# Performance work log

Measured on AMD Instinct MI355X. Metric: run time of the kernel, lower is better.

## Reference

```python
import jax, jax.numpy as jnp
import numpy as np

N_TOKENS = 1024
HIDDEN = 2048
N_EXPERTS = 16
MOE_INTER = 1024
TOP_K = 6
N_GROUP = 4
TOPK_GROUP = 2
N_SHARED = 2
ROUTED_SCALING = 2.5
RENORM = True
CAPACITY = 1024  # >> N_TOKENS*TOP_K/N_EXPERTS = 384; overflow probability negligible


def setup_inputs() -> dict:
    key = jax.random.key(0)
    ks = jax.random.split(key, 7)
    s = 0.02
    return {
        'hidden_states': jax.random.normal(ks[0], (N_TOKENS, HIDDEN), jnp.float32),
        'gate_w': jax.random.normal(ks[1], (N_EXPERTS, HIDDEN), jnp.float32) * s,
        'gate_bias': jax.random.normal(ks[2], (N_EXPERTS,), jnp.float32) * s,
        'w_gate_up': jax.random.normal(ks[3], (N_EXPERTS, HIDDEN, 2 * MOE_INTER), jnp.float32) * s,
        'w_down': jax.random.normal(ks[4], (N_EXPERTS, MOE_INTER, HIDDEN), jnp.float32) * s,
        'shared_w_gate_up': jax.random.normal(ks[5], (HIDDEN, 2 * N_SHARED * MOE_INTER), jnp.float32) * s,
        'shared_w_down': jax.random.normal(ks[6], (N_SHARED * MOE_INTER, HIDDEN), jnp.float32) * s,
    }


def _swiglu(gu):
    # npu_swiglu with activate_left=True: silu(first half) * second half
    g, u = jnp.split(gu, 2, axis=-1)
    return jax.nn.silu(g) * u


def reference(hidden_states, gate_w, gate_bias, w_gate_up, w_down, shared_w_gate_up, shared_w_down):
    x = hidden_states
    N, H = x.shape
    E, K, C = N_EXPERTS, TOP_K, CAPACITY
    P = N * K  # number of (token, slot) pairs

    # ---- MoEGate: router logits + noaux_tc grouped top-k ----
    logits = x @ gate_w.T                              # [N, E]
    scores = jax.nn.sigmoid(logits)                    # sigmoid scoring (noaux_tc)
    s_corr = scores + gate_bias[None, :]
    sg = s_corr.reshape(N, N_GROUP, E // N_GROUP)
    group_scores = jax.lax.top_k(sg, 2)[0].sum(-1)     # top-2 sum per group [N, G]
    _, gidx = jax.lax.top_k(group_scores, TOPK_GROUP)
    gmask = jnp.sum(jax.nn.one_hot(gidx, N_GROUP, dtype=jnp.float32), axis=1) > 0
    masked = jnp.where(gmask[:, :, None], sg, -jnp.inf).reshape(N, E)
    _, topk_ids = jax.lax.top_k(masked, K)             # [N, K]
    w = jnp.take_along_axis(scores, topk_ids, axis=-1)  # weights from original scores
    if RENORM:
        w = w / jnp.sum(w, axis=-1, keepdims=True)
    w = w * ROUTED_SCALING

    # ---- dispatch: fixed-capacity buffers per expert ----
    flat_e = topk_ids.reshape(P)
    onehot = jax.nn.one_hot(flat_e, E, dtype=jnp.int32)
    pos = jnp.cumsum(onehot, axis=0)[jnp.arange(P), flat_e] - 1  # slot within expert
    valid = pos < C
    buf = jnp.full((E, C), P, jnp.int32).at[flat_e, jnp.clip(pos, 0, C - 1)].set(
        jnp.where(valid, jnp.arange(P, dtype=jnp.int32), P))
    tok = jnp.where(buf < P, buf // K, N)              # token index per slot, N = pad
    x_pad = jnp.concatenate([x, jnp.zeros((1, H), x.dtype)], axis=0)
    xe = x_pad[tok]                                    # [E, C, H]

    # ---- grouped expert GEMMs (SwiGLU MLP per expert) ----
    h = jnp.einsum('ech,ehi->eci', xe, w_gate_up)      # [E, C, 2I]
    y = jnp.einsum('eci,eih->ech', _swiglu(h), w_down)  # [E, C, H]

    # ---- combine: weighted scatter-add back to tokens ----
    w_pad = jnp.concatenate([w.reshape(P), jnp.zeros((1,), w.dtype)])
    pw = w_pad[jnp.where(buf < P, buf, P)]             # [E, C]
    routed = jnp.zeros((N + 1, H), x.dtype).at[tok].add(y * pw[:, :, None])[:N]

    # ---- shared experts (reduce_results=False, fused add) ----
    shared = _swiglu(x @ shared_w_gate_up) @ shared_w_down
    return routed + shared
```

## Files before the change

### kernel.cpp

```cpp
#include <hip/hip_runtime.h>
#include <hip/hip_bf16.h>
#include <math.h>

typedef __attribute__((ext_vector_type(8))) short bf16x8;
typedef __attribute__((ext_vector_type(4))) float f32x4;

#define N_TOK 1024
#define HID   2048
#define NEXP  16
#define NE2   18
#define INTER 1024
#define TOPK  6
#define CAP   1024

__device__ __forceinline__ unsigned short f2bf(float f) {
  unsigned u = __builtin_bit_cast(unsigned, f);
  u += 0x7fffu + ((u >> 16) & 1u);
  return (unsigned short)(u >> 16);
}
__device__ __forceinline__ float b2f(short s) {
  unsigned u = ((unsigned)(unsigned short)s) << 16;
  return __builtin_bit_cast(float, u);
}
__device__ __forceinline__ void gll16(const void* g, void* l) {
  __builtin_amdgcn_global_load_lds(
      (const __attribute__((address_space(1))) unsigned int*)g,
      (__attribute__((address_space(3))) unsigned int*)l, 16, 0, 0);
}
__device__ __forceinline__ void xcd_remap(int& bx, int& by, int& bz) {
  int gx = gridDim.x, gy = gridDim.y;
  int nwg = gx * gy * (int)gridDim.z;
  int lid = bx + gx * (by + gy * bz);
  int q = nwg >> 3, r = nwg & 7;
  int xcd = lid & 7, i = lid >> 3;
  int swz = (xcd < r ? xcd * (q + 1) : r * (q + 1) + (xcd - r) * q) + i;
  bx = swz % gx; int t2 = swz / gx; by = t2 % gy; bz = t2 / gy;
}

__global__ __launch_bounds__(256) void router_k(
    const float* __restrict__ x, const float* __restrict__ gw,
    const float* __restrict__ gb, int* __restrict__ counts,
    int* __restrict__ tok_list, int* __restrict__ meta,
    float* __restrict__ pwt, unsigned short* __restrict__ x_bf)
{
  const int t   = blockIdx.x;
  const int tid = threadIdx.x;
  __shared__ float xrow[HID];
  __shared__ float logits[NEXP];

  for (int i = tid; i < HID; i += 256) {
    float v = x[(size_t)t * HID + i];
    xrow[i] = v;
    x_bf[(size_t)t * HID + i] = f2bf(v);
  }
  __syncthreads();

  const int w = tid >> 6, lane = tid & 63;
  for (int s = 0; s < 4; ++s) {
    int e = w * 4 + s;
    const float* g = gw + (size_t)e * HID;
    float p = 0.f;
    for (int i = lane; i < HID; i += 64) p += xrow[i] * g[i];
    for (int off = 32; off; off >>= 1) p += __shfl_down(p, off);
    if (lane == 0) logits[e] = p;
  }
  __syncthreads();

  if (tid == 0) {
    float sc[NEXP], scorr[NEXP];
    for (int e = 0; e < NEXP; ++e) {
      float s1 = 1.f / (1.f + expf(-logits[e]));
      sc[e] = s1; scorr[e] = s1 + gb[e];
    }
    float gs[4];
    for (int g = 0; g < 4; ++g) {
      float m1 = -1e30f, m2 = -1e30f;
      for (int j = 0; j < 4; ++j) {
        float v = scorr[g * 4 + j];
        if (v > m1) { m2 = m1; m1 = v; } else if (v > m2) m2 = v;
      }
      gs[g] = m1 + m2;
    }
    int g1 = 0;
    for (int g = 1; g < 4; ++g) if (gs[g] > gs[g1]) g1 = g;
    int g2 = -1;
    for (int g = 0; g < 4; ++g) { if (g == g1) continue; if (g2 < 0 || gs[g] > gs[g2]) g2 = g; }

    bool taken[NEXP];
    for (int e = 0; e < NEXP; ++e) taken[e] = false;
    int ids[TOPK]; float wv[TOPK]; float wsum = 0.f;
    for (int k = 0; k < TOPK; ++k) {
      int best = -1; float bv = -1e30f;
      for (int e = 0; e < NEXP; ++e) {
        int grp = e >> 2;
        if (grp != g1 && grp != g2) continue;
        if (taken[e]) continue;
        if (scorr[e] > bv) { bv = scorr[e]; best = e; }
      }
      taken[best] = true; ids[k] = best; wv[k] = sc[best]; wsum += sc[best];
    }
    float inv = 2.5f / wsum;
    for (int k = 0; k < TOPK; ++k) {
      int e = ids[k];
      int slot = atomicAdd(&counts[e], 1);
      tok_list[e * CAP + slot] = t;
      meta[t * TOPK + k] = (e << 16) | slot;
      pwt[t * TOPK + k] = wv[k] * inv;
    }
  }
}

template<int MODE>
__global__ __launch_bounds__(256, 2) void gemm_fw_k(
    const unsigned short* __restrict__ A, int lda, size_t a_estride,
    const float* __restrict__ Wr, const float* __restrict__ Ws, int K,
    const int* __restrict__ counts, const int* __restrict__ tok_list,
    unsigned short* __restrict__ outb, int out_ld, size_t out_estride)
{
  int bx = blockIdx.x, by = blockIdx.y, bz = blockIdx.z;
  xcd_remap(bx, by, bz);
  const int e  = bz;
  const int m0 = by * 128;
  const int M  = (e < 16) ? counts[e] : N_TOK;
  if (m0 >= M) return;
  const int n0 = bx * (MODE == 0 ? 64 : 128);

  __shared__ __align__(16) unsigned short Al[2][128 * 64];
  __shared__ __align__(16) unsigned short Bl[2][128 * 64];

  const int tid = threadIdx.x, lane = tid & 63, wid = tid >> 6;
  const int wm = wid >> 1, wn = wid & 1, l15 = lane & 15, hi = lane >> 4;

  const unsigned short* Ap = A + (size_t)e * a_estride;

  const unsigned short* asrc[4]; int aoff[4];
  #pragma unroll
  for (int i = 0; i < 4; ++i) {
    int c = tid + 256 * i;
    int r = c >> 3, s = c & 7, sl = s ^ (r & 7);
    int slot = m0 + r;
    int row;
    if (MODE == 0) row = (e < 16) ? ((slot < M) ? tok_list[e * CAP + slot] : 0) : slot;
    else           row = slot;
    asrc[i] = Ap + (size_t)row * lda + sl * 8;
    aoff[i] = c * 16;
  }

  const int nq = tid & 31, kb8 = tid >> 5;
  const float* bp; int ldw;
  {
    int n_ = nq * 4;
    if (MODE == 0) {
      if (e < 16) {
        size_t col = (n_ < 64) ? (size_t)(n0 + n_) : (size_t)(1024 + n0 + n_ - 64);
        bp = Wr + (size_t)e * HID * (2 * INTER) + col; ldw = 2 * INTER;
      } else {
        int j = e - 16;
        size_t col = (n_ < 64) ? (size_t)(j * 1024 + n0 + n_)
                               : (size_t)(2048 + j * 1024 + n0 + n_ - 64);
        bp = Ws + col; ldw = 4096;
      }
    } else {
      bp = ((e < 16) ? Wr + (size_t)e * INTER * HID
                     : Ws + (size_t)(e - 16) * INTER * HID) + (n0 + n_);
      ldw = HID;
    }
    bp += (size_t)(kb8 * 8) * ldw;
  }
  int bwoff[4];
  #pragma unroll
  for (int j = 0; j < 4; ++j)
    bwoff[j] = (nq * 4 + j) * 128 + ((kb8 ^ (nq & 7) ^ (j << 1)) << 4);

  int bn[4];
  if (MODE == 0) { bn[0] = wn*32; bn[1] = wn*32+16; bn[2] = 64+wn*32; bn[3] = 80+wn*32; }
  else           { bn[0] = wn*64; bn[1] = wn*64+16; bn[2] = wn*64+32; bn[3] = wn*64+48; }

  f32x4 acc[4][4];
  #pragma unroll
  for (int a0 = 0; a0 < 4; ++a0)
    #pragma unroll
    for (int b0 = 0; b0 < 4; ++b0) acc[a0][b0] = (f32x4){0.f, 0.f, 0.f, 0.f};

  float4 bf4[8];
  #define LOADB(kt)                                                         \
    _Pragma("unroll")                                                       \
    for (int i = 0; i < 8; ++i)                                             \
      bf4[i] = *(const float4*)(bp + (size_t)((kt) + i) * ldw);
  #define WRITEB(Bb)                                                        \
    _Pragma("unroll")                                                       \
    for (int j = 0; j < 4; ++j) {                                           \
      unsigned w4[4];                                                       \
      _Pragma("unroll")                                                     \
      for (int q2 = 0; q2 < 4; ++q2) {                                      \
        float lo  = ((const float*)(bf4 + 2 * q2))[j];                      \
        float hi2 = ((const float*)(bf4 + 2 * q2 + 1))[j];                  \
        unsigned rr;                                                        \
        asm("v_cvt_pk_bf16_f32 %0, %1, %2" : "=v"(rr) : "v"(lo), "v"(hi2)); \
        w4[q2] = rr;                                                        \
      }                                                                     \
      *(uint4*)((char*)(Bb) + bwoff[j]) = *(uint4*)w4;                      \
    }

  LOADB(0)
  #pragma unroll
  for (int i = 0; i < 4; ++i) gll16(asrc[i], (char*)Al[0] + aoff[i]);
  asm volatile("s_waitcnt vmcnt(0)" ::: "memory");
  WRITEB(Bl[0])
  __syncthreads();

  const int nt = K >> 6;
  int p = 0;
  for (int t = 0; t < nt; ++t) {
    const bool pf = (t + 1 < nt);
    if (pf) {
      const int kt1 = (t + 1) << 6;
      #pragma unroll
      for (int i = 0; i < 4; ++i)
        gll16(asrc[i] + kt1, (char*)Al[p ^ 1] + aoff[i]);
      LOADB(kt1)
    }

    const char* Ab = (const char*)Al[p];
    const char* Bb = (const char*)Bl[p];
    #pragma unroll
    for (int kk = 0; kk < 64; kk += 32) {
      bf16x8 af[4], bv[4];
      #pragma unroll
      for (int mi = 0; mi < 4; ++mi) {
        int r = wm * 64 + mi * 16 + l15;
        int off = (r * 128 + (kk + hi * 8) * 2) ^ ((r & 7) << 4);
        af[mi] = *(const bf16x8*)(Ab + off);
      }
      #pragma unroll
      for (int ni = 0; ni < 4; ++ni) {
        int r = bn[ni] + l15;
        int slot = (kk >> 3) + hi;
        int off = r * 128 + ((slot ^ ((r >> 2) & 7) ^ ((r & 3) << 1)) << 4);
        bv[ni] = *(const bf16x8*)(Bb + off);
      }
      #pragma unroll
      for (int mi = 0; mi < 4; ++mi)
        #pragma unroll
        for (int ni = 0; ni < 4; ++ni)
          acc[mi][ni] = __builtin_amdgcn_mfma_f32_16x16x32_bf16(af[mi], bv[ni], acc[mi][ni], 0, 0, 0);
    }

    if (pf) {
      asm volatile("s_waitcnt vmcnt(0)" ::: "memory");
      WRITEB(Bl[p ^ 1])
    }
    __syncthreads();
    p ^= 1;
  }
  #undef LOADB
  #undef WRITEB

  const int rbase = hi * 4;
  if (MODE == 0) {
    #pragma unroll
    for (int mi = 0; mi < 4; ++mi)
      #pragma unroll
      for (int rr = 0; rr < 4; ++rr) {
        int slot = m0 + wm * 64 + mi * 16 + rbase + rr;
        if (slot >= M) continue;
        #pragma unroll
        for (int j = 0; j < 2; ++j) {
          float g = acc[mi][j][rr], u = acc[mi][j + 2][rr];
          float sv = g / (1.f + expf(-g)) * u;
          int col = n0 + wn * 32 + j * 16 + l15;
          outb[(size_t)e * out_estride + (size_t)slot * out_ld + col] = f2bf(sv);
        }
      }
  } else {
    #pragma unroll
    for (int mi = 0; mi < 4; ++mi)
      #pragma unroll
      for (int rr = 0; rr < 4; ++rr) {
        int slot = m0 + wm * 64 + mi * 16 + rbase + rr;
        if (slot >= M) continue;
        unsigned short* row = outb + (size_t)e * out_estride + (size_t)slot * out_ld;
        #pragma unroll
        for (int ni = 0; ni < 4; ++ni)
          row[n0 + bn[ni] + l15] = f2bf(acc[mi][ni][rr]);
      }
  }
}

__global__ __launch_bounds__(256) void combine_k(
    const unsigned short* __restrict__ ybuf, const int* __restrict__ meta,
    const float* __restrict__ pwt, float* __restrict__ out)
{
  const int t = blockIdx.x;
  const int c0 = threadIdx.x * 8;
  float acc[8];
  {
    bf16x8 v0 = *(const bf16x8*)(ybuf + ((size_t)16 * CAP + t) * HID + c0);
    bf16x8 v1 = *(const bf16x8*)(ybuf + ((size_t)17 * CAP + t) * HID + c0);
    #pragma unroll
    for (int j = 0; j < 8; ++j) acc[j] = b2f(v0[j]) + b2f(v1[j]);
  }
  #pragma unroll
  for (int k = 0; k < TOPK; ++k) {
    int m = meta[t * TOPK + k];
    float w = pwt[t * TOPK + k];
    int e = m >> 16, s = m & 0xffff;
    bf16x8 v = *(const bf16x8*)(ybuf + ((size_t)e * CAP + s) * HID + c0);
    #pragma unroll
    for (int j = 0; j < 8; ++j) acc[j] += w * b2f(v[j]);
  }
  float4* o = (float4*)(out + (size_t)t * HID + c0);
  o[0] = make_float4(acc[0], acc[1], acc[2], acc[3]);
  o[1] = make_float4(acc[4], acc[5], acc[6], acc[7]);
}

extern "C" void kernel_launch(void* const* d_in, const int* in_sizes, int n_in,
                              void* d_out, int out_size, void* d_ws, size_t ws_size,
                              hipStream_t stream) {
  const float* x   = (const float*)d_in[0];
  const float* gw  = (const float*)d_in[1];
  const float* gb  = (const float*)d_in[2];
  const float* wgu = (const float*)d_in[3];
  const float* wd  = (const float*)d_in[4];
  const float* sgu = (const float*)d_in[5];
  const float* sd  = (const float*)d_in[6];
  float* out = (float*)d_out;

  char* ws = (char*)d_ws;
  int*   counts   = (int*)ws;
  int*   tok_list = (int*)(ws + 256);
  int*   meta     = (int*)(ws + 256 + 65536);
  float* pwt      = (float*)(ws + 256 + 65536 + 24576);
  unsigned short* x_bf = (unsigned short*)(ws + 128 * 1024);
  unsigned short* act  = x_bf + (size_t)N_TOK * HID;
  unsigned short* ybuf = act + (size_t)NE2 * CAP * INTER;
  const size_t need = (size_t)((char*)(ybuf + (size_t)NE2 * CAP * HID) - ws);
  if (ws_size < need) return;

  hipMemsetAsync(counts, 0, 256, stream);
  router_k<<<N_TOK, 256, 0, stream>>>(x, gw, gb, counts, tok_list, meta, pwt, x_bf);

  gemm_fw_k<0><<<dim3(INTER / 64, CAP / 128, NE2), 256, 0, stream>>>(
      x_bf, HID, 0, wgu, sgu, HID, counts, tok_list,
      act, INTER, (size_t)CAP * INTER);
  gemm_fw_k<1><<<dim3(HID / 128, CAP / 128, NE2), 256, 0, stream>>>(
      act, INTER, (size_t)CAP * INTER, wd, sd, INTER, counts, nullptr,
      ybuf, HID, (size_t)CAP * HID);

  combine_k<<<N_TOK, 256, 0, stream>>>(ybuf, meta, pwt, out);
}
```

Before: 479.0 us.

## Deepen B-operand prefetch to two register stages with partial vmcnt waits

Restructures the GEMM main loop to keep two register buffers of fp32 B tiles in flight, loading tile t+2 while tile t+1 is converted and written to LDS. Each wait drops from vmcnt(0) to vmcnt(8), so global loads overlap the MFMA compute instead of stalling on it. The loop is unrolled by two, and sched_barriers pin the instruction order. It costs more VGPRs, which may lower occupancy, and relies on nt being even and on redundant clamped loads past the end.

```diff
diff --git a/kernel.cpp b/kernel.cpp
--- a/kernel.cpp
+++ b/kernel.cpp
@@ -182,79 +182,99 @@
     #pragma unroll
     for (int b0 = 0; b0 < 4; ++b0) acc[a0][b0] = (f32x4){0.f, 0.f, 0.f, 0.f};
 
-  float4 bf4[8];
-  #define LOADB(kt)                                                         \
+  float4 rb0[8], rb1[8];
+
+  #define LOADB(rb, kt)                                                     \
     _Pragma("unroll")                                                       \
     for (int i = 0; i < 8; ++i)                                             \
-      bf4[i] = *(const float4*)(bp + (size_t)((kt) + i) * ldw);
-  #define WRITEB(Bb)                                                        \
+      rb[i] = *(const float4*)(bp + (size_t)((kt) + i) * ldw);
+  #define WRITEB(rb, Bb)                                                    \
     _Pragma("unroll")                                                       \
     for (int j = 0; j < 4; ++j) {                                           \
       unsigned w4[4];                                                       \
       _Pragma("unroll")                                                     \
       for (int q2 = 0; q2 < 4; ++q2) {                                      \
-        float lo  = ((const float*)(bf4 + 2 * q2))[j];                      \
-        float hi2 = ((const float*)(bf4 + 2 * q2 + 1))[j];                  \
+        float lo  = ((const float*)(rb + 2 * q2))[j];                       \
+        float hi2 = ((const float*)(rb + 2 * q2 + 1))[j];                   \
         unsigned rr;                                                        \
         asm("v_cvt_pk_bf16_f32 %0, %1, %2" : "=v"(rr) : "v"(lo), "v"(hi2)); \
         w4[q2] = rr;                                                        \
       }                                                                     \
       *(uint4*)((char*)(Bb) + bwoff[j]) = *(uint4*)w4;                      \
     }
-
-  LOADB(0)
+  #define COMPUTE(Ab, Bb)                                                   \
+    _Pragma("unroll")                                                       \
+    for (int kk = 0; kk < 64; kk += 32) {                                   \
+      bf16x8 af[4], bv[4];                                                  \
+      _Pragma("unroll")                                                     \
+      for (int mi = 0; mi < 4; ++mi) {                                      \
+        int r = wm * 64 + mi * 16 + l15;                                    \
+        int off = (r * 128 + (kk + hi * 8) * 2) ^ ((r & 7) << 4);           \
+        af[mi] = *(const bf16x8*)((const char*)(Ab) + off);                 \
+      }                                                                     \
+      _Pragma("unroll")                                                     \
+      for (int ni = 0; ni < 4; ++ni) {                                      \
+        int r = bn[ni] + l15;                                               \
+        int slot = (kk >> 3) + hi;                                          \
+        int off = r * 128 + ((slot ^ ((r >> 2) & 7) ^ ((r & 3) << 1)) << 4);\
+        bv[ni] = *(const bf16x8*)((const char*)(Bb) + off);                 \
+      }                                                                     \
+      _Pragma("unroll")                                                     \
+      for (int mi = 0; mi < 4; ++mi)                                        \
+        _Pragma("unroll")                                                   \
+        for (int ni = 0; ni < 4; ++ni)                                      \
+          acc[mi][ni] = __builtin_amdgcn_mfma_f32_16x16x32_bf16(            \
+              af[mi], bv[ni], acc[mi][ni], 0, 0, 0);                        \
+    }
+
+  const int nt = K >> 6;
+  const int LT = (nt - 1) << 6;
+
+  LOADB(rb0, 0)
   #pragma unroll
   for (int i = 0; i < 4; ++i) gll16(asrc[i], (char*)Al[0] + aoff[i]);
-  asm volatile("s_waitcnt vmcnt(0)" ::: "memory");
-  WRITEB(Bl[0])
-  __syncthreads();
-
-  const int nt = K >> 6;
-  int p = 0;
-  for (int t = 0; t < nt; ++t) {
-    const bool pf = (t + 1 < nt);
-    if (pf) {
-      const int kt1 = (t + 1) << 6;
+  WRITEB(rb0, Bl[0])
+  LOADB(rb0, 64 < K ? 64 : LT)
+  asm volatile("s_waitcnt vmcnt(8)" ::: "memory");
+  asm volatile("s_waitcnt lgkmcnt(0)" ::: "memory");
+  __builtin_amdgcn_s_barrier();
+  __builtin_amdgcn_sched_barrier(0);
+
+  for (int t = 0; t < nt; t += 2) {
+    {
+      int ka = (t + 1 < nt) ? (t + 1) << 6 : LT;
+      int kb = (t + 2 < nt) ? (t + 2) << 6 : LT;
       #pragma unroll
-      for (int i = 0; i < 4; ++i)
-        gll16(asrc[i] + kt1, (char*)Al[p ^ 1] + aoff[i]);
-      LOADB(kt1)
-    }
-
-    const char* Ab = (const char*)Al[p];
-    const char* Bb = (const char*)Bl[p];
-    #pragma unroll
-    for (int kk = 0; kk < 64; kk += 32) {
-      bf16x8 af[4], bv[4];
+      for (int i = 0; i < 4; ++i) gll16(asrc[i] + ka, (char*)Al[1] + aoff[i]);
+      LOADB(rb1, kb)
+      __builtin_amdgcn_sched_barrier(0);
+      COMPUTE(Al[0], Bl[0])
+      WRITEB(rb0, Bl[1])
+      __builtin_amdgcn_sched_barrier(0);
+      asm volatile("s_waitcnt vmcnt(8)" ::: "memory");
+      asm volatile("s_waitcnt lgkmcnt(0)" ::: "memory");
+      __builtin_amdgcn_s_barrier();
+      __builtin_amdgcn_sched_barrier(0);
+    }
+    {
+      int ka = (t + 2 < nt) ? (t + 2) << 6 : LT;
+      int kb = (t + 3 < nt) ? (t + 3) << 6 : LT;
       #pragma unroll
-      for (int mi = 0; mi < 4; ++mi) {
-        int r = wm * 64 + mi * 16 + l15;
-        int off = (r * 128 + (kk + hi * 8) * 2) ^ ((r & 7) << 4);
-        af[mi] = *(const bf16x8*)(Ab + off);
-      }
-      #pragma unroll
-      for (int ni = 0; ni < 4; ++ni) {
-        int r = bn[ni] + l15;
-        int slot = (kk >> 3) + hi;
-        int off = r * 128 + ((slot ^ ((r >> 2) & 7) ^ ((r & 3) << 1)) << 4);
-        bv[ni] = *(const bf16x8*)(Bb + off);
-      }
-      #pragma unroll
-      for (int mi = 0; mi < 4; ++mi)
-        #pragma unroll
-        for (int ni = 0; ni < 4; ++ni)
-          acc[mi][ni] = __builtin_amdgcn_mfma_f32_16x16x32_bf16(af[mi], bv[ni], acc[mi][ni], 0, 0, 0);
-    }
-
-    if (pf) {
-      asm volatile("s_waitcnt vmcnt(0)" ::: "memory");
-      WRITEB(Bl[p ^ 1])
-    }
-    __syncthreads();
-    p ^= 1;
+      for (int i = 0; i < 4; ++i) gll16(asrc[i] + ka, (char*)Al[0] + aoff[i]);
+      LOADB(rb0, kb)
+      __builtin_amdgcn_sched_barrier(0);
+      COMPUTE(Al[1], Bl[1])
+      WRITEB(rb1, Bl[0])
+      __builtin_amdgcn_sched_barrier(0);
+      asm volatile("s_waitcnt vmcnt(8)" ::: "memory");
+      asm volatile("s_waitcnt lgkmcnt(0)" ::: "memory");
+      __builtin_amdgcn_s_barrier();
+      __builtin_amdgcn_sched_barrier(0);
+    }
   }
   #undef LOADB
   #undef WRITEB
+  #undef COMPUTE
 
   const int rbase = hi * 4;
   if (MODE == 0) {
```

Result: faster. 468.0 us (-2.3%).
